# Kernel optimization log

Measured on AMD Instinct MI355X. Metric: run time of the kernel, lower is better.

Reference implementation:

```python
import jax, jax.numpy as jnp
import numpy as np

N_HEADS = 16
HEAD_DIM = 64
HIDDEN = 1024
LN_EPS = 1e-6

def setup_inputs() -> dict:
    key = jax.random.key(0)
    ks = jax.random.split(key, 8)
    B, L, H = 2, 2048, HIDDEN
    s = 1.0 / np.sqrt(H)
    return {
        "q": jax.random.normal(ks[0], (B, L, H), jnp.float32),
        "k": jax.random.normal(ks[1], (B, L, H), jnp.float32),
        "v": jax.random.normal(ks[2], (B, L, H), jnp.float32),
        "w_qs": jax.random.normal(ks[3], (H, N_HEADS * HEAD_DIM), jnp.float32) * s,
        "w_ks": jax.random.normal(ks[4], (H, N_HEADS * HEAD_DIM), jnp.float32) * s,
        "w_vs": jax.random.normal(ks[5], (H, N_HEADS * HEAD_DIM), jnp.float32) * s,
        "w_fc": jax.random.normal(ks[6], (N_HEADS * HEAD_DIM, H), jnp.float32) * s,
        "ln_gamma": jnp.ones((H,), jnp.float32),
        "ln_beta": jnp.zeros((H,), jnp.float32),
    }

def reference(q, k, v, w_qs, w_ks, w_vs, w_fc, ln_gamma, ln_beta):
    B, Lq, H = q.shape
    residual = q
    # projections -> [B, heads, L, head_dim]
    qh = (q @ w_qs).reshape(B, Lq, N_HEADS, HEAD_DIM).transpose(0, 2, 1, 3)
    kh = (k @ w_ks).reshape(B, -1, N_HEADS, HEAD_DIM).transpose(0, 2, 1, 3)
    vh = (v @ w_vs).reshape(B, -1, N_HEADS, HEAD_DIM).transpose(0, 2, 1, 3)
    temp = jnp.asarray(HEAD_DIM ** 0.5, qh.dtype)
    scores = jnp.einsum("bhqd,bhkd->bhqk", qh / temp, kh)  # [B,H,Lq,Lk]
    attn = jax.nn.softmax(scores, axis=-1)  # dropout = identity (eval)
    out = jnp.einsum("bhqk,bhkd->bhqd", attn, vh)
    out = out.transpose(0, 2, 1, 3).reshape(B, Lq, N_HEADS * HEAD_DIM)
    out = out @ w_fc  # dropout = identity (eval)
    x = residual + out
    mu = jnp.mean(x, axis=-1, keepdims=True)
    var = jnp.var(x, axis=-1, keepdims=True)
    y = (x - mu) * jax.lax.rsqrt(var + LN_EPS) * ln_gamma + ln_beta
    return (y, attn)
```

## Files before the change

### kernel.cpp

```cpp
#include <hip/hip_runtime.h>
#include <stdint.h>

#define NHEADS 16
#define HDIM   64
#define HID    1024
#define SEQ    2048
#define NB     2

typedef short s16x8 __attribute__((ext_vector_type(8)));
typedef float f32x4 __attribute__((ext_vector_type(4)));

__device__ __forceinline__ short f2bf(float f) {
  union { float f; unsigned u; } x; x.f = f;
  unsigned r = (x.u + 0x7FFFu + ((x.u >> 16) & 1u)) >> 16;
  return (short)r;
}

__device__ __forceinline__ void gload16(const void* g, void* l) {
  __builtin_amdgcn_global_load_lds(
      (const __attribute__((address_space(1))) unsigned int*)g,
      (__attribute__((address_space(3))) unsigned int*)l, 16, 0, 0);
}

__global__ __launch_bounds__(256, 4)
void proj_gemm(const unsigned short* __restrict__ qb, const unsigned short* __restrict__ kb,
               const unsigned short* __restrict__ vb,
               const unsigned short* __restrict__ wqt, const unsigned short* __restrict__ wkt,
               const unsigned short* __restrict__ wvt,
               unsigned short* __restrict__ Qh, unsigned short* __restrict__ Kh,
               unsigned short* __restrict__ Vt)
{
  __shared__ unsigned short As[64 * 64];
  __shared__ unsigned short Bs[128 * 64];
  const int tid = threadIdx.x, lane = tid & 63, w = tid >> 6;
  const int lg = lane >> 4, ll = lane & 15;
  const int wm = w & 1, wn = w >> 1;
  const int z = blockIdx.z;
  const int m0 = blockIdx.x * 64, n0 = blockIdx.y * 128;
  const int xorv = (ll & 7) << 4;

  const unsigned short* A  = z == 0 ? qb : z == 1 ? kb : vb;
  const unsigned short* Bt = z == 0 ? wqt : z == 1 ? wkt : wvt;
  const float alpha = z == 0 ? 0.125f : 1.0f;

  f32x4 acc[2][4];
#pragma unroll
  for (int m = 0; m < 2; ++m)
#pragma unroll
    for (int n = 0; n < 4; ++n) acc[m][n] = (f32x4)0.f;

  int rA[2], cA[2], rB[4], cB[4];
#pragma unroll
  for (int c = 0; c < 2; ++c) {
    const int b = (w * 2 + c) * 1024 + lane * 16;
    rA[c] = b >> 7; cA[c] = (b & 127) ^ ((rA[c] & 7) << 4);
  }
#pragma unroll
  for (int c = 0; c < 4; ++c) {
    const int b = (w * 4 + c) * 1024 + lane * 16;
    rB[c] = b >> 7; cB[c] = (b & 127) ^ ((rB[c] & 7) << 4);
  }

  for (int k0 = 0; k0 < HID; k0 += 64) {
    __syncthreads();
#pragma unroll
    for (int c = 0; c < 2; ++c)
      gload16((const char*)A + ((((size_t)(m0 + rA[c]) * HID + k0) << 1) + cA[c]),
              (char*)As + (w * 2 + c) * 1024);
#pragma unroll
    for (int c = 0; c < 4; ++c)
      gload16((const char*)Bt + ((((size_t)(n0 + rB[c]) * HID + k0) << 1) + cB[c]),
              (char*)Bs + (w * 4 + c) * 1024);
    __syncthreads();
#pragma unroll
    for (int kk = 0; kk < 2; ++kk) {
      const int cb2 = kk * 64 + lg * 16;
      s16x8 a[2], b[4];
#pragma unroll
      for (int m = 0; m < 2; ++m)
        a[m] = *(const s16x8*)((const char*)As + ((((wm * 32 + m * 16 + ll) << 7) + cb2) ^ xorv));
#pragma unroll
      for (int n = 0; n < 4; ++n)
        b[n] = *(const s16x8*)((const char*)Bs + ((((wn * 64 + n * 16 + ll) << 7) + cb2) ^ xorv));
#pragma unroll
      for (int m = 0; m < 2; ++m)
#pragma unroll
        for (int n = 0; n < 4; ++n)
          acc[m][n] = __builtin_amdgcn_mfma_f32_16x16x32_bf16(a[m], b[n], acc[m][n], 0, 0, 0);
    }
  }

#pragma unroll
  for (int m = 0; m < 2; ++m)
#pragma unroll
    for (int n = 0; n < 4; ++n)
#pragma unroll
      for (int r = 0; r < 4; ++r) {
        const int row = m0 + wm * 32 + m * 16 + lg * 4 + r;
        const int col = n0 + wn * 64 + n * 16 + ll;
        const int bb = row >> 11, l = row & (SEQ - 1);
        const int h = col >> 6, d = col & (HDIM - 1);
        const unsigned short o = (unsigned short)f2bf(acc[m][n][r] * alpha);
        if (z < 2) {
          unsigned short* out = z == 0 ? Qh : Kh;
          out[(((size_t)(bb * NHEADS + h) * SEQ + l) * HDIM) + d] = o;
        } else {
          Vt[(((size_t)(bb * NHEADS + h) * HDIM + d) * SEQ) + l] = o;
        }
      }
}

__global__ __launch_bounds__(256, 4)
void fc_gemm(const unsigned short* __restrict__ A, const unsigned short* __restrict__ Bt,
             float* __restrict__ C, const float* __restrict__ resid)
{
  __shared__ unsigned short As[64 * 64];
  __shared__ unsigned short Bs[128 * 64];
  const int tid = threadIdx.x, lane = tid & 63, w = tid >> 6;
  const int lg = lane >> 4, ll = lane & 15;
  const int wm = w & 1, wn = w >> 1;
  const int m0 = blockIdx.x * 64, n0 = blockIdx.y * 128;
  const int xorv = (ll & 7) << 4;

  f32x4 acc[2][4];
#pragma unroll
  for (int m = 0; m < 2; ++m)
#pragma unroll
    for (int n = 0; n < 4; ++n) acc[m][n] = (f32x4)0.f;

  int rA[2], cA[2], rB[4], cB[4];
#pragma unroll
  for (int c = 0; c < 2; ++c) {
    const int b = (w * 2 + c) * 1024 + lane * 16;
    rA[c] = b >> 7; cA[c] = (b & 127) ^ ((rA[c] & 7) << 4);
  }
#pragma unroll
  for (int c = 0; c < 4; ++c) {
    const int b = (w * 4 + c) * 1024 + lane * 16;
    rB[c] = b >> 7; cB[c] = (b & 127) ^ ((rB[c] & 7) << 4);
  }

  for (int k0 = 0; k0 < HID; k0 += 64) {
    __syncthreads();
#pragma unroll
    for (int c = 0; c < 2; ++c)
      gload16((const char*)A + ((((size_t)(m0 + rA[c]) * HID + k0) << 1) + cA[c]),
              (char*)As + (w * 2 + c) * 1024);
#pragma unroll
    for (int c = 0; c < 4; ++c)
      gload16((const char*)Bt + ((((size_t)(n0 + rB[c]) * HID + k0) << 1) + cB[c]),
              (char*)Bs + (w * 4 + c) * 1024);
    __syncthreads();
#pragma unroll
    for (int kk = 0; kk < 2; ++kk) {
      const int cb2 = kk * 64 + lg * 16;
      s16x8 a[2], b[4];
#pragma unroll
      for (int m = 0; m < 2; ++m)
        a[m] = *(const s16x8*)((const char*)As + ((((wm * 32 + m * 16 + ll) << 7) + cb2) ^ xorv));
#pragma unroll
      for (int n = 0; n < 4; ++n)
        b[n] = *(const s16x8*)((const char*)Bs + ((((wn * 64 + n * 16 + ll) << 7) + cb2) ^ xorv));
#pragma unroll
      for (int m = 0; m < 2; ++m)
#pragma unroll
        for (int n = 0; n < 4; ++n)
          acc[m][n] = __builtin_amdgcn_mfma_f32_16x16x32_bf16(a[m], b[n], acc[m][n], 0, 0, 0);
    }
  }

#pragma unroll
  for (int m = 0; m < 2; ++m)
#pragma unroll
    for (int n = 0; n < 4; ++n)
#pragma unroll
      for (int r = 0; r < 4; ++r) {
        const int row = m0 + wm * 32 + m * 16 + lg * 4 + r;
        const int col = n0 + wn * 64 + n * 16 + ll;
        const size_t idx = (size_t)row * HID + col;
        C[idx] = acc[m][n][r] + resid[idx];
      }
}

__global__ __launch_bounds__(256, 3)
void fused_attn(const unsigned short* __restrict__ Qh,
                const unsigned short* __restrict__ Kh,
                const unsigned short* __restrict__ Vt,
                float* __restrict__ attn,
                unsigned short* __restrict__ Ofc)
{
  __shared__ unsigned short Ks[128 * 64];
  __shared__ unsigned short Vs[64 * 128];
  __shared__ unsigned short Ps[128][72];
  const int tid = threadIdx.x, lane = tid & 63, w = tid >> 6;
  const int lg = lane >> 4, ll = lane & 15;
  const int xorv = (ll & 7) << 4;

  const int lin = blockIdx.y * gridDim.x + blockIdx.x;
  const int lin2 = (lin & 7) * 64 + (lin >> 3);
  const int z = lin2 >> 4, qb = lin2 & 15;
  const int bb = z >> 4, h = z & 15;
  const int m0 = qb * 128;

  const unsigned short* Qz = Qh + (size_t)z * SEQ * HDIM;
  const unsigned short* Kz = Kh + (size_t)z * SEQ * HDIM;
  const unsigned short* Vz = Vt + (size_t)z * HDIM * SEQ;
  float* Az = attn + (size_t)z * SEQ * SEQ;

  int rK[4], cbK[4], rV[4], cbV[4];
#pragma unroll
  for (int c = 0; c < 4; ++c) {
    const int b = (w * 4 + c) * 1024 + lane * 16;
    rK[c] = b >> 7; cbK[c] = (b & 127) ^ ((rK[c] & 7) << 4);
    rV[c] = b >> 8; cbV[c] = (b & 255) ^ ((rV[c] & 7) << 4);
  }

  s16x8 qf[2][2];
#pragma unroll
  for (int m = 0; m < 2; ++m)
#pragma unroll
    for (int kk = 0; kk < 2; ++kk)
      qf[m][kk] = *(const s16x8*)(Qz + (size_t)(m0 + w * 32 + m * 16 + ll) * HDIM
                                  + kk * 32 + lg * 8);

  float sml[8];
#pragma unroll
  for (int i = 0; i < 8; ++i) sml[i] = 0.f;

  for (int j = 0; j < 16; ++j) {
    __syncthreads();
#pragma unroll
    for (int c = 0; c < 4; ++c)
      gload16((const char*)Kz + ((((size_t)(j * 128 + rK[c]) * HDIM) << 1) + cbK[c]),
              (char*)Ks + (w * 4 + c) * 1024);
    __syncthreads();
    f32x4 s[2][8];
#pragma unroll
    for (int m = 0; m < 2; ++m)
#pragma unroll
      for (int n = 0; n < 8; ++n) s[m][n] = (f32x4)0.f;
#pragma unroll
    for (int kk = 0; kk < 2; ++kk) {
      const int cb2 = kk * 64 + lg * 16;
      s16x8 bk[8];
#pragma unroll
      for (int n = 0; n < 8; ++n)
        bk[n] = *(const s16x8*)((const char*)Ks + ((((n * 16 + ll) << 7) + cb2) ^ xorv));
#pragma unroll
      for (int m = 0; m < 2; ++m)
#pragma unroll
        for (int n = 0; n < 8; ++n)
          s[m][n] = __builtin_amdgcn_mfma_f32_16x16x32_bf16(qf[m][kk], bk[n], s[m][n], 0, 0, 0);
    }
#pragma unroll
    for (int m = 0; m < 2; ++m)
#pragma unroll
      for (int r = 0; r < 4; ++r) {
        const int i = m * 4 + r;
#pragma unroll
        for (int n = 0; n < 8; ++n) sml[i] += __expf(s[m][n][r]);
      }
  }
  float inv[8];
#pragma unroll
  for (int i = 0; i < 8; ++i) {
    float su = sml[i];
#pragma unroll
    for (int off = 1; off < 16; off <<= 1) su += __shfl_xor(su, off, 64);
    inv[i] = 1.0f / su;
  }

  f32x4 ao[2][4];
#pragma unroll
  for (int m = 0; m < 2; ++m)
#pragma unroll
    for (int n = 0; n < 4; ++n) ao[m][n] = (f32x4)0.f;

  for (int j = 0; j < 16; ++j) {
    __syncthreads();
#pragma unroll
    for (int c = 0; c < 4; ++c) {
      gload16((const char*)Kz + ((((size_t)(j * 128 + rK[c]) * HDIM) << 1) + cbK[c]),
              (char*)Ks + (w * 4 + c) * 1024);
      gload16((const char*)Vz + ((((size_t)rV[c] * SEQ + j * 128) << 1) + cbV[c]),
              (char*)Vs + (w * 4 + c) * 1024);
    }
    __syncthreads();
    f32x4 s[2][8];
#pragma unroll
    for (int m = 0; m < 2; ++m)
#pragma unroll
      for (int n = 0; n < 8; ++n) s[m][n] = (f32x4)0.f;
#pragma unroll
    for (int kk = 0; kk < 2; ++kk) {
      const int cb2 = kk * 64 + lg * 16;
      s16x8 bk[8];
#pragma unroll
      for (int n = 0; n < 8; ++n)
        bk[n] = *(const s16x8*)((const char*)Ks + ((((n * 16 + ll) << 7) + cb2) ^ xorv));
#pragma unroll
      for (int m = 0; m < 2; ++m)
#pragma unroll
        for (int n = 0; n < 8; ++n)
          s[m][n] = __builtin_amdgcn_mfma_f32_16x16x32_bf16(qf[m][kk], bk[n], s[m][n], 0, 0, 0);
    }
#pragma unroll
    for (int h2 = 0; h2 < 2; ++h2) {
#pragma unroll
      for (int m = 0; m < 2; ++m)
#pragma unroll
        for (int r = 0; r < 4; ++r) {
          const int i = m * 4 + r;
          const int rowl = w * 32 + m * 16 + lg * 4 + r;
          float* dst = Az + (size_t)(m0 + rowl) * SEQ + j * 128 + h2 * 64 + ll;
#pragma unroll
          for (int nn = 0; nn < 4; ++nn) {
            const float p = __expf(s[m][h2 * 4 + nn][r]) * inv[i];
            __builtin_nontemporal_store(p, dst + nn * 16);
            Ps[rowl][nn * 16 + ll] = (unsigned short)f2bf(p);
          }
        }
#pragma unroll
      for (int kkl = 0; kkl < 2; ++kkl) {
        const int cb2v = (h2 * 2 + kkl) * 64 + lg * 16;
        s16x8 pa[2], vbf[4];
#pragma unroll
        for (int m = 0; m < 2; ++m)
          pa[m] = *(const s16x8*)&Ps[w * 32 + m * 16 + ll][kkl * 32 + lg * 8];
#pragma unroll
        for (int n = 0; n < 4; ++n)
          vbf[n] = *(const s16x8*)((const char*)Vs + ((((n * 16 + ll) << 8) + cb2v) ^ xorv));
#pragma unroll
        for (int m = 0; m < 2; ++m)
#pragma unroll
          for (int n = 0; n < 4; ++n)
            ao[m][n] = __builtin_amdgcn_mfma_f32_16x16x32_bf16(pa[m], vbf[n], ao[m][n], 0, 0, 0);
      }
    }
  }

#pragma unroll
  for (int m = 0; m < 2; ++m)
#pragma unroll
    for (int n = 0; n < 4; ++n)
#pragma unroll
      for (int r = 0; r < 4; ++r) {
        const int qrow = m0 + w * 32 + m * 16 + lg * 4 + r;
        const int d = n * 16 + ll;
        Ofc[((size_t)bb * SEQ + qrow) * HID + h * HDIM + d] =
            (unsigned short)f2bf(ao[m][n][r]);
      }
}

__global__ __launch_bounds__(256)
void cast3_bf16(const float* __restrict__ s0, const float* __restrict__ s1,
                const float* __restrict__ s2, unsigned short* __restrict__ d0,
                unsigned short* __restrict__ d1, unsigned short* __restrict__ d2)
{
  const float* s = blockIdx.y == 0 ? s0 : blockIdx.y == 1 ? s1 : s2;
  unsigned short* d = blockIdx.y == 0 ? d0 : blockIdx.y == 1 ? d1 : d2;
  const size_t i = ((size_t)blockIdx.x * 256 + threadIdx.x) * 8;
  const float4 f0 = ((const float4*)(s + i))[0];
  const float4 f1 = ((const float4*)(s + i))[1];
  s16x8 o;
  o[0] = f2bf(f0.x); o[1] = f2bf(f0.y); o[2] = f2bf(f0.z); o[3] = f2bf(f0.w);
  o[4] = f2bf(f1.x); o[5] = f2bf(f1.y); o[6] = f2bf(f1.z); o[7] = f2bf(f1.w);
  *(s16x8*)(d + i) = o;
}

__global__ __launch_bounds__(256)
void transpose_cast_w4(const float* __restrict__ s0, const float* __restrict__ s1,
                       const float* __restrict__ s2, const float* __restrict__ s3,
                       unsigned short* __restrict__ d0, unsigned short* __restrict__ d1,
                       unsigned short* __restrict__ d2, unsigned short* __restrict__ d3)
{
  const float* src = blockIdx.z == 0 ? s0 : blockIdx.z == 1 ? s1 : blockIdx.z == 2 ? s2 : s3;
  unsigned short* dst = blockIdx.z == 0 ? d0 : blockIdx.z == 1 ? d1 : blockIdx.z == 2 ? d2 : d3;
  __shared__ float t[32][33];
  const int tx = threadIdx.x & 31, ty = threadIdx.x >> 5;
  const int x0 = blockIdx.x * 32, y0 = blockIdx.y * 32;
#pragma unroll
  for (int i = 0; i < 4; ++i) {
    const int r = ty + i * 8;
    t[r][tx] = src[(size_t)(y0 + r) * HID + (x0 + tx)];
  }
  __syncthreads();
#pragma unroll
  for (int i = 0; i < 4; ++i) {
    const int r = ty + i * 8;
    dst[(size_t)(x0 + r) * HID + (y0 + tx)] = (unsigned short)f2bf(t[tx][r]);
  }
}

__global__ __launch_bounds__(256)
void ln_kernel(const float* __restrict__ x, const float* __restrict__ gamma,
               const float* __restrict__ beta, float* __restrict__ y)
{
  const int tid = threadIdx.x;
  const size_t row = blockIdx.x;
  const float4 v = ((const float4*)(x + row * HID))[tid];
  float s = v.x + v.y + v.z + v.w;
  float q = v.x * v.x + v.y * v.y + v.z * v.z + v.w * v.w;
#pragma unroll
  for (int off = 32; off; off >>= 1) {
    s += __shfl_xor(s, off, 64);
    q += __shfl_xor(q, off, 64);
  }
  __shared__ float ps[4], pq[4];
  const int wid = tid >> 6, lane = tid & 63;
  if (lane == 0) { ps[wid] = s; pq[wid] = q; }
  __syncthreads();
  const float ts = ps[0] + ps[1] + ps[2] + ps[3];
  const float tq = pq[0] + pq[1] + pq[2] + pq[3];
  const float mu = ts * (1.0f / HID);
  const float var = tq * (1.0f / HID) - mu * mu;
  const float rs = rsqrtf(var + 1e-6f);
  const float4 g = ((const float4*)gamma)[tid];
  const float4 bb = ((const float4*)beta)[tid];
  float4 o;
  o.x = (v.x - mu) * rs * g.x + bb.x;
  o.y = (v.y - mu) * rs * g.y + bb.y;
  o.z = (v.z - mu) * rs * g.z + bb.z;
  o.w = (v.w - mu) * rs * g.w + bb.w;
  ((float4*)(y + row * HID))[tid] = o;
}

extern "C" void kernel_launch(void* const* d_in, const int* in_sizes, int n_in,
                              void* d_out, int out_size, void* d_ws, size_t ws_size,
                              hipStream_t stream)
{
  (void)in_sizes; (void)n_in; (void)out_size; (void)ws_size;
  const float* q     = (const float*)d_in[0];
  const float* k     = (const float*)d_in[1];
  const float* v     = (const float*)d_in[2];
  const float* w_qs  = (const float*)d_in[3];
  const float* w_ks  = (const float*)d_in[4];
  const float* w_vs  = (const float*)d_in[5];
  const float* w_fc  = (const float*)d_in[6];
  const float* gamma = (const float*)d_in[7];
  const float* beta  = (const float*)d_in[8];

  char* ws = (char*)d_ws;
  unsigned short* wqt = (unsigned short*)(ws);
  unsigned short* wkt = (unsigned short*)(ws + ((size_t)2 << 20));
  unsigned short* wvt = (unsigned short*)(ws + ((size_t)4 << 20));
  unsigned short* wft = (unsigned short*)(ws + ((size_t)6 << 20));
  unsigned short* qb  = (unsigned short*)(ws + ((size_t)8 << 20));
  unsigned short* kb  = (unsigned short*)(ws + ((size_t)16 << 20));
  unsigned short* vb  = (unsigned short*)(ws + ((size_t)24 << 20));
  unsigned short* Qh  = (unsigned short*)(ws + ((size_t)32 << 20));
  unsigned short* Kh  = (unsigned short*)(ws + ((size_t)40 << 20));
  unsigned short* Vt  = (unsigned short*)(ws + ((size_t)48 << 20));
  unsigned short* Ofc = qb;
  float*          xres = (float*)(ws + ((size_t)16 << 20));

  float* y_out = (float*)d_out;
  float* attn  = (float*)d_out + (size_t)NB * SEQ * HID;

  const dim3 b256(256, 1, 1);

  transpose_cast_w4<<<dim3(32, 32, 4), b256, 0, stream>>>(
      w_qs, w_ks, w_vs, w_fc, wqt, wkt, wvt, wft);
  cast3_bf16<<<dim3(2048, 3, 1), b256, 0, stream>>>(q, k, v, qb, kb, vb);

  proj_gemm<<<dim3(64, 8, 3), b256, 0, stream>>>(qb, kb, vb, wqt, wkt, wvt, Qh, Kh, Vt);

  fused_attn<<<dim3(16, 32, 1), b256, 0, stream>>>(Qh, Kh, Vt, attn, Ofc);

  fc_gemm<<<dim3(64, 8, 1), b256, 0, stream>>>(Ofc, wft, xres, q);

  ln_kernel<<<dim3(NB * SEQ, 1, 1), b256, 0, stream>>>(xres, gamma, beta, y_out);
}
```

Measured before the change: 256.5 us.

## Fuse input bf16 cast into projection GEMM and vectorize attention-prob stores

Removes the separate cast3_bf16 kernel: proj_gemm now reads the fp32 q/k/v directly, converts to bf16 in registers and writes the result into swizzled LDS. The M tile grows from 64 to 128 to amortize the fp32 reads, with occupancy lowered to 3 waves per SIMD. In fused_attn, the attention probabilities are no longer written as scattered scalar fp32 stores. They are read back from the bf16 P tile in LDS and written as 16-byte nontemporal vectors, and the Ps row is padded to 80. The written attn values are now bf16-rounded, which may reduce output precision.

```diff
diff --git a/kernel.cpp b/kernel.cpp
--- a/kernel.cpp
+++ b/kernel.cpp
@@ -15,6 +15,10 @@
   unsigned r = (x.u + 0x7FFFu + ((x.u >> 16) & 1u)) >> 16;
   return (short)r;
 }
+__device__ __forceinline__ float bf2f(unsigned short u) {
+  union { unsigned u; float f; } x; x.u = ((unsigned)u) << 16;
+  return x.f;
+}
 
 __device__ __forceinline__ void gload16(const void* g, void* l) {
   __builtin_amdgcn_global_load_lds(
@@ -22,41 +26,40 @@
       (__attribute__((address_space(3))) unsigned int*)l, 16, 0, 0);
 }
 
-__global__ __launch_bounds__(256, 4)
-void proj_gemm(const unsigned short* __restrict__ qb, const unsigned short* __restrict__ kb,
-               const unsigned short* __restrict__ vb,
+__global__ __launch_bounds__(256, 3)
+void proj_gemm(const float* __restrict__ q, const float* __restrict__ k,
+               const float* __restrict__ v,
                const unsigned short* __restrict__ wqt, const unsigned short* __restrict__ wkt,
                const unsigned short* __restrict__ wvt,
                unsigned short* __restrict__ Qh, unsigned short* __restrict__ Kh,
                unsigned short* __restrict__ Vt)
 {
-  __shared__ unsigned short As[64 * 64];
+  __shared__ unsigned short As[128 * 64];
   __shared__ unsigned short Bs[128 * 64];
   const int tid = threadIdx.x, lane = tid & 63, w = tid >> 6;
   const int lg = lane >> 4, ll = lane & 15;
   const int wm = w & 1, wn = w >> 1;
   const int z = blockIdx.z;
-  const int m0 = blockIdx.x * 64, n0 = blockIdx.y * 128;
+  const int m0 = blockIdx.x * 128, n0 = blockIdx.y * 128;
   const int xorv = (ll & 7) << 4;
 
-  const unsigned short* A  = z == 0 ? qb : z == 1 ? kb : vb;
+  const float* Af = z == 0 ? q : z == 1 ? k : v;
   const unsigned short* Bt = z == 0 ? wqt : z == 1 ? wkt : wvt;
   const float alpha = z == 0 ? 0.125f : 1.0f;
 
-  f32x4 acc[2][4];
-#pragma unroll
-  for (int m = 0; m < 2; ++m)
+  f32x4 acc[4][4];
+#pragma unroll
+  for (int m = 0; m < 4; ++m)
 #pragma unroll
     for (int n = 0; n < 4; ++n) acc[m][n] = (f32x4)0.f;
 
-  int rA[2], cA[2], rB[4], cB[4];
-#pragma unroll
-  for (int c = 0; c < 2; ++c) {
-    const int b = (w * 2 + c) * 1024 + lane * 16;
-    rA[c] = b >> 7; cA[c] = (b & 127) ^ ((rA[c] & 7) << 4);
-  }
+  int rA[4], k8A[4], dwA[4];
+  int rB[4], cB[4];
 #pragma unroll
   for (int c = 0; c < 4; ++c) {
+    const int s = tid + c * 256;
+    rA[c] = s >> 3; k8A[c] = s & 7;
+    dwA[c] = ((rA[c] << 7) + (k8A[c] << 4)) ^ ((rA[c] & 7) << 4);
     const int b = (w * 4 + c) * 1024 + lane * 16;
     rB[c] = b >> 7; cB[c] = (b & 127) ^ ((rB[c] & 7) << 4);
   }
@@ -64,26 +67,30 @@
   for (int k0 = 0; k0 < HID; k0 += 64) {
     __syncthreads();
 #pragma unroll
-    for (int c = 0; c < 2; ++c)
-      gload16((const char*)A + ((((size_t)(m0 + rA[c]) * HID + k0) << 1) + cA[c]),
-              (char*)As + (w * 2 + c) * 1024);
-#pragma unroll
-    for (int c = 0; c < 4; ++c)
+    for (int c = 0; c < 4; ++c) {
+      const float* src = Af + (size_t)(m0 + rA[c]) * HID + k0 + k8A[c] * 8;
+      const float4 f0 = ((const float4*)src)[0];
+      const float4 f1 = ((const float4*)src)[1];
+      s16x8 sa;
+      sa[0] = f2bf(f0.x); sa[1] = f2bf(f0.y); sa[2] = f2bf(f0.z); sa[3] = f2bf(f0.w);
+      sa[4] = f2bf(f1.x); sa[5] = f2bf(f1.y); sa[6] = f2bf(f1.z); sa[7] = f2bf(f1.w);
+      *(s16x8*)((char*)As + dwA[c]) = sa;
       gload16((const char*)Bt + ((((size_t)(n0 + rB[c]) * HID + k0) << 1) + cB[c]),
               (char*)Bs + (w * 4 + c) * 1024);
+    }
     __syncthreads();
 #pragma unroll
     for (int kk = 0; kk < 2; ++kk) {
       const int cb2 = kk * 64 + lg * 16;
-      s16x8 a[2], b[4];
-#pragma unroll
-      for (int m = 0; m < 2; ++m)
-        a[m] = *(const s16x8*)((const char*)As + ((((wm * 32 + m * 16 + ll) << 7) + cb2) ^ xorv));
+      s16x8 a[4], b[4];
+#pragma unroll
+      for (int m = 0; m < 4; ++m)
+        a[m] = *(const s16x8*)((const char*)As + ((((wm * 64 + m * 16 + ll) << 7) + cb2) ^ xorv));
 #pragma unroll
       for (int n = 0; n < 4; ++n)
         b[n] = *(const s16x8*)((const char*)Bs + ((((wn * 64 + n * 16 + ll) << 7) + cb2) ^ xorv));
 #pragma unroll
-      for (int m = 0; m < 2; ++m)
+      for (int m = 0; m < 4; ++m)
 #pragma unroll
         for (int n = 0; n < 4; ++n)
           acc[m][n] = __builtin_amdgcn_mfma_f32_16x16x32_bf16(a[m], b[n], acc[m][n], 0, 0, 0);
@@ -91,12 +98,12 @@
   }
 
 #pragma unroll
-  for (int m = 0; m < 2; ++m)
+  for (int m = 0; m < 4; ++m)
 #pragma unroll
     for (int n = 0; n < 4; ++n)
 #pragma unroll
       for (int r = 0; r < 4; ++r) {
-        const int row = m0 + wm * 32 + m * 16 + lg * 4 + r;
+        const int row = m0 + wm * 64 + m * 16 + lg * 4 + r;
         const int col = n0 + wn * 64 + n * 16 + ll;
         const int bb = row >> 11, l = row & (SEQ - 1);
         const int h = col >> 6, d = col & (HDIM - 1);
@@ -191,7 +198,7 @@
 {
   __shared__ unsigned short Ks[128 * 64];
   __shared__ unsigned short Vs[64 * 128];
-  __shared__ unsigned short Ps[128][72];
+  __shared__ unsigned short Ps[128][80];
   const int tid = threadIdx.x, lane = tid & 63, w = tid >> 6;
   const int lg = lane >> 4, ll = lane & 15;
   const int xorv = (ll & 7) << 4;
@@ -312,13 +319,10 @@
         for (int r = 0; r < 4; ++r) {
           const int i = m * 4 + r;
           const int rowl = w * 32 + m * 16 + lg * 4 + r;
-          float* dst = Az + (size_t)(m0 + rowl) * SEQ + j * 128 + h2 * 64 + ll;
-#pragma unroll
-          for (int nn = 0; nn < 4; ++nn) {
-            const float p = __expf(s[m][h2 * 4 + nn][r]) * inv[i];
-            __builtin_nontemporal_store(p, dst + nn * 16);
-            Ps[rowl][nn * 16 + ll] = (unsigned short)f2bf(p);
-          }
+#pragma unroll
+          for (int nn = 0; nn < 4; ++nn)
+            Ps[rowl][nn * 16 + ll] =
+                (unsigned short)f2bf(__expf(s[m][h2 * 4 + nn][r]) * inv[i]);
         }
 #pragma unroll
       for (int kkl = 0; kkl < 2; ++kkl) {
@@ -335,6 +339,21 @@
 #pragma unroll
           for (int n = 0; n < 4; ++n)
             ao[m][n] = __builtin_amdgcn_mfma_f32_16x16x32_bf16(pa[m], vbf[n], ao[m][n], 0, 0, 0);
+      }
+#pragma unroll
+      for (int vv = 0; vv < 4; ++vv) {
+        const int slot = vv * 64 + lane;
+        const int srow = slot >> 3, k8 = slot & 7;
+        const s16x8 pw = *(const s16x8*)&Ps[w * 32 + srow][k8 * 8];
+        f32x4 o0, o1;
+        o0[0] = bf2f((unsigned short)pw[0]); o0[1] = bf2f((unsigned short)pw[1]);
+        o0[2] = bf2f((unsigned short)pw[2]); o0[3] = bf2f((unsigned short)pw[3]);
+        o1[0] = bf2f((unsigned short)pw[4]); o1[1] = bf2f((unsigned short)pw[5]);
+        o1[2] = bf2f((unsigned short)pw[6]); o1[3] = bf2f((unsigned short)pw[7]);
+        f32x4* dst = (f32x4*)(Az + (size_t)(m0 + w * 32 + srow) * SEQ
+                              + j * 128 + h2 * 64 + k8 * 8);
+        __builtin_nontemporal_store(o0, dst);
+        __builtin_nontemporal_store(o1, dst + 1);
       }
     }
   }
@@ -350,22 +369,6 @@
         Ofc[((size_t)bb * SEQ + qrow) * HID + h * HDIM + d] =
             (unsigned short)f2bf(ao[m][n][r]);
       }
-}
-
-__global__ __launch_bounds__(256)
-void cast3_bf16(const float* __restrict__ s0, const float* __restrict__ s1,
-                const float* __restrict__ s2, unsigned short* __restrict__ d0,
-                unsigned short* __restrict__ d1, unsigned short* __restrict__ d2)
-{
-  const float* s = blockIdx.y == 0 ? s0 : blockIdx.y == 1 ? s1 : s2;
-  unsigned short* d = blockIdx.y == 0 ? d0 : blockIdx.y == 1 ? d1 : d2;
-  const size_t i = ((size_t)blockIdx.x * 256 + threadIdx.x) * 8;
-  const float4 f0 = ((const float4*)(s + i))[0];
-  const float4 f1 = ((const float4*)(s + i))[1];
-  s16x8 o;
-  o[0] = f2bf(f0.x); o[1] = f2bf(f0.y); o[2] = f2bf(f0.z); o[3] = f2bf(f0.w);
-  o[4] = f2bf(f1.x); o[5] = f2bf(f1.y); o[6] = f2bf(f1.z); o[7] = f2bf(f1.w);
-  *(s16x8*)(d + i) = o;
 }
 
 __global__ __launch_bounds__(256)
@@ -445,14 +448,11 @@
   unsigned short* wkt = (unsigned short*)(ws + ((size_t)2 << 20));
   unsigned short* wvt = (unsigned short*)(ws + ((size_t)4 << 20));
   unsigned short* wft = (unsigned short*)(ws + ((size_t)6 << 20));
-  unsigned short* qb  = (unsigned short*)(ws + ((size_t)8 << 20));
-  unsigned short* kb  = (unsigned short*)(ws + ((size_t)16 << 20));
-  unsigned short* vb  = (unsigned short*)(ws + ((size_t)24 << 20));
-  unsigned short* Qh  = (unsigned short*)(ws + ((size_t)32 << 20));
-  unsigned short* Kh  = (unsigned short*)(ws + ((size_t)40 << 20));
-  unsigned short* Vt  = (unsigned short*)(ws + ((size_t)48 << 20));
-  unsigned short* Ofc = qb;
-  float*          xres = (float*)(ws + ((size_t)16 << 20));
+  unsigned short* Qh  = (unsigned short*)(ws + ((size_t)8 << 20));
+  unsigned short* Kh  = (unsigned short*)(ws + ((size_t)16 << 20));
+  unsigned short* Vt  = (unsigned short*)(ws + ((size_t)24 << 20));
+  unsigned short* Ofc = (unsigned short*)(ws + ((size_t)32 << 20));
+  float*          xres = (float*)(ws + ((size_t)40 << 20));
 
   float* y_out = (float*)d_out;
   float* attn  = (float*)d_out + (size_t)NB * SEQ * HID;
@@ -461,9 +461,8 @@
 
   transpose_cast_w4<<<dim3(32, 32, 4), b256, 0, stream>>>(
       w_qs, w_ks, w_vs, w_fc, wqt, wkt, wvt, wft);
-  cast3_bf16<<<dim3(2048, 3, 1), b256, 0, stream>>>(q, k, v, qb, kb, vb);
-
-  proj_gemm<<<dim3(64, 8, 3), b256, 0, stream>>>(qb, kb, vb, wqt, wkt, wvt, Qh, Kh, Vt);
+
+  proj_gemm<<<dim3(32, 8, 3), b256, 0, stream>>>(q, k, v, wqt, wkt, wvt, Qh, Kh, Vt);
 
   fused_attn<<<dim3(16, 32, 1), b256, 0, stream>>>(Qh, Kh, Vt, attn, Ofc);
 
```

Result: slower. 387.8 us (+51.2%).
